# Kernel tuning notes

Measured on AMD Instinct MI355X. Metric: run time of the kernel, lower is better.

Reference implementation:

```python
import jax, jax.numpy as jnp
import numpy as np

B, D, H, G, WR = 8192, 1024, 1024, 2, 64
URANKS = [64, 64]


def setup_inputs() -> dict:
    key = jax.random.key(0)
    ks = jax.random.split(key, 12)
    s = 0.1
    return {
        "x": jax.random.normal(ks[0], (B, D), jnp.float32),
        "h": jax.random.normal(ks[1], (B, H), jnp.float32),
        "c": jax.random.normal(ks[2], (B, H), jnp.float32),
        "dia_x": s * jax.random.normal(ks[3], (1, D), jnp.float32),
        "dia_h": s * jax.random.normal(ks[4], (1, H), jnp.float32),
        "Ux": s * jax.random.normal(ks[5], (D, WR), jnp.float32),
        "Vx": s * jax.random.normal(ks[6], (4 * H, WR), jnp.float32),
        "Uh_0": s * jax.random.normal(ks[7], (G, H // G, URANKS[0]), jnp.float32),
        "Vh_0": s * jax.random.normal(ks[8], (G, URANKS[0], 4 * (H // G)), jnp.float32),
        "Uh_1": s * jax.random.normal(ks[9], (G, H // G, URANKS[1]), jnp.float32),
        "Vh_1": s * jax.random.normal(ks[10], (G, URANKS[1], 4 * (H // G)), jnp.float32),
        "bias_x": jnp.ones((1, 4 * H), jnp.float32),
        "bias_h": jnp.ones((1, 4 * H), jnp.float32),
    }


def reference(x, h, c, dia_x, dia_h, Ux, Vx, Uh_0, Vh_0, Uh_1, Vh_1, bias_x, bias_h):
    Bn, Dn = x.shape
    Hn = h.shape[1]
    g = Uh_0.shape[0]
    Hg = Hn // g
    r0 = Uh_0.shape[2]

    # diagonal (vector-multiplication) paths, x-part zero-padded to hidden width
    vm_x = jnp.pad(dia_x * x, ((0, 0), (0, Hn - Dn)))          # [B, H]
    vm_h = dia_h * h                                           # [B, H]

    # low-rank input projection
    lowered_x = (x @ Ux) @ Vx.T                                # [B, 4H]

    # refined diagonal corrections subtracted from the low-rank outputs
    Vx4 = Vx.reshape(4, Hn, -1)[:, :Dn, :]                     # [4, D, wR]
    coef_x = jnp.sum(Ux[None, :, :] * Vx4, axis=-1)            # [4, D]
    vm_refined_x = jnp.pad(x[:, None, :] * coef_x[None], ((0, 0), (0, 0), (0, Hn - Dn))).reshape(Bn, 4 * Hn)

    Uh0f = Uh_0.reshape(Hn, r0)                                # [H, r0]
    Vh0f = jnp.transpose(Vh_0, (0, 2, 1)).reshape(4 * Hn, r0).reshape(4, Hn, r0)
    coef_h = jnp.sum(Uh0f[None, :, :] * Vh0f, axis=-1)         # [4, H]
    vm_refined_h = (h[:, None, :] * coef_h[None]).reshape(Bn, 4 * Hn)

    gx = lowered_x - vm_refined_x + bias_x
    xi, xf, xo, xn = jnp.split(gx, 4, axis=1)

    # grouped low-rank recurrent projection with cyclic group permutation
    hv = h.reshape(Bn, g, Hg)
    Uhs = [Uh_0, Uh_1]
    Vhs = [Vh_0, Vh_1]
    g_h = jnp.zeros((Bn, 4 * Hn), x.dtype)
    for i in range(g):
        idx = np.roll(np.arange(g), -i)                        # static permutation
        hp = hv[:, idx, :]                                     # [B, g, H/g]
        t = jnp.einsum('bgn,gnr->bgr', hp, Uhs[i])             # [B, g, r_i]
        t = jnp.einsum('bgr,grm->bgm', t, Vhs[i])              # [B, g, 4H/g]
        g_h = g_h + t.reshape(Bn, 4 * Hn)

    gh = g_h - vm_refined_h + bias_h
    hf, hi, hn, ho = jnp.split(gh, 4, axis=1)                  # note gate order differs from x

    base = vm_x + vm_h
    inputgate = jax.nn.sigmoid(xi + hi + base)
    forgetgate = jax.nn.sigmoid(xf + hf + base)
    outputgate = jax.nn.sigmoid(xo + ho + base)
    newgate = jnp.tanh(xn + hn + base)

    c_next = forgetgate * c + inputgate * newgate
    h_next = outputgate * jnp.tanh(c_next)
    return (h_next, c_next)
```

## Files before the change

### kernel.cpp

```cpp
#include <hip/hip_runtime.h>


typedef _Float16 half8 __attribute__((ext_vector_type(8)));
typedef _Float16 half4v __attribute__((ext_vector_type(4)));
typedef float f32x4 __attribute__((ext_vector_type(4)));

#define WS_TA    0
#define WS_TB    3145728
#define WS_U1F   6291456
#define WS_UH1F  6422528
#define WS_W2    6684672
#define WS_CX    8257536
#define WS_CH    8273920
#define WS_BB    8290304

__global__ __launch_bounds__(256) void prep_kernel(
    const float* __restrict__ Ux, const float* __restrict__ Vx,
    const float* __restrict__ Uh0, const float* __restrict__ Vh0,
    const float* __restrict__ Uh1, const float* __restrict__ Vh1,
    const float* __restrict__ dia_x, const float* __restrict__ dia_h,
    const float* __restrict__ bias_x, const float* __restrict__ bias_h,
    _Float16* __restrict__ U1f, _Float16* __restrict__ Uh1f,
    _Float16* __restrict__ W2f, float* __restrict__ cx,
    float* __restrict__ ch, float* __restrict__ bb)
{
    int e = blockIdx.x * 256 + threadIdx.x;
    if (e < 8192) {
        int lane = e & 63, ks = (e >> 6) & 31, ct = e >> 11;
        int l15 = lane & 15, quad = lane >> 4;
        half8 v8;
        #pragma unroll
        for (int jj = 0; jj < 8; ++jj) {
            int k = ks * 32 + quad * 8 + jj;
            v8[jj] = (_Float16)Ux[k * 64 + ct * 16 + l15];
        }
        *(half8*)&U1f[(size_t)e * 8] = v8;
    } else if (e < 24576) {
        int t = e - 8192;
        int lane = t & 63, ks = (t >> 6) & 15, ct = (t >> 10) & 3, j = t >> 12;
        int l15 = lane & 15, quad = lane >> 4;
        const float* src = (j & 1) ? Uh1 : Uh0;
        int g = j >> 1;
        half8 v8;
        #pragma unroll
        for (int jj = 0; jj < 8; ++jj) {
            int k = ks * 32 + quad * 8 + jj;
            v8[jj] = (_Float16)src[(g * 512 + k) * 64 + ct * 16 + l15];
        }
        *(half8*)&Uh1f[(size_t)t * 8] = v8;
    } else if (e < 122880) {
        int t = e - 24576;
        int lane = t & 63;
        int ksq  = (t >> 6) % 6;
        int ct   = (t / 384) & 63;
        int g01  = (t / 24576) & 1;
        int s    = t / 49152;
        int l15 = lane & 15, quad = lane >> 4;
        int k = ct * 16 + l15;
        int jx = s * 2 + g01;
        int m = (g01 == 0) ? (1024 + k) : k;
        half8 v8;
        #pragma unroll
        for (int jj = 0; jj < 8; ++jj) {
            int kk = ksq * 32 + quad * 8 + jj;
            int r = kk & 63, sect = kk >> 6;
            float val;
            if (sect == 0)      val = Vx[(jx * 1024 + k) * 64 + r];
            else if (sect == 1) val = Vh0[(s * 64 + r) * 2048 + m];
            else                val = Vh1[(s * 64 + r) * 2048 + m];
            v8[jj] = (_Float16)val;
        }
        *(half8*)&W2f[(size_t)t * 8] = v8;
    } else if (e < 126976) {
        int t = e - 122880; int q = t >> 10; int k = t & 1023;
        int jh = q ^ 1;
        int fh = jh * 1024 + k; int g = fh >> 11; int m = fh & 2047;
        float sx = 0.f, sh = 0.f;
        for (int r = 0; r < 64; ++r) {
            sx += Ux[k * 64 + r] * Vx[(q * 1024 + k) * 64 + r];
            sh += Uh0[k * 64 + r] * Vh0[(g * 64 + r) * 2048 + m];
        }
        cx[t] = dia_x[k] - sx;
        ch[t] = dia_h[k] - sh;
        bb[t] = bias_x[q * 1024 + k] + bias_h[jh * 1024 + k];
    }
}

__global__ __launch_bounds__(256) void s1_kernel(
    const float* __restrict__ x, const float* __restrict__ h,
    const _Float16* __restrict__ U1f, const _Float16* __restrict__ Uh1f,
    _Float16* __restrict__ Ta, _Float16* __restrict__ Tb)
{
    __shared__ __align__(16) _Float16 Ash[16][520];

    const int job = blockIdx.y;
    const int b0 = blockIdx.x * 16;
    const int tid = threadIdx.x;
    const int w = tid >> 6, l = tid & 63, l15 = l & 15, quad = l >> 4;

    f32x4 acc0 = {}, acc1 = {};
    const int nkc = (job == 0) ? 2 : 1;
    const float* src = (job == 0) ? x : h;

    for (int kc = 0; kc < nkc; ++kc) {
        const int koff = (job == 2) ? 512 : kc * 512;
        #pragma unroll
        for (int ii = 0; ii < 8; ++ii) {
            int idx = tid + ii * 256;
            int row = idx >> 7, c4 = idx & 127;
            float4 f = *(const float4*)&src[(size_t)(b0 + row) * 1024 + koff + c4 * 4];
            half4v p;
            p[0] = (_Float16)f.x; p[1] = (_Float16)f.y;
            p[2] = (_Float16)f.z; p[3] = (_Float16)f.w;
            *(half4v*)&Ash[row][c4 * 4] = p;
        }
        __syncthreads();
        if (job == 0) {
            const _Float16* bp = U1f + ((size_t)(w * 32 + kc * 16) * 64 + l) * 8;
            #pragma unroll
            for (int ks = 0; ks < 16; ++ks) {
                half8 a = *(const half8*)&Ash[l15][ks * 32 + quad * 8];
                half8 b = *(const half8*)(bp + (size_t)ks * 512);
                acc0 = __builtin_amdgcn_mfma_f32_16x16x32_f16(a, b, acc0, 0, 0, 0);
            }
        } else {
            const int j0 = (job == 1) ? 0 : 1;
            const int j1 = (job == 1) ? 3 : 2;
            const _Float16* bp0 = Uh1f + ((size_t)((j0 * 4 + w) * 16) * 64 + l) * 8;
            const _Float16* bp1 = Uh1f + ((size_t)((j1 * 4 + w) * 16) * 64 + l) * 8;
            #pragma unroll
            for (int ks = 0; ks < 16; ++ks) {
                half8 a = *(const half8*)&Ash[l15][ks * 32 + quad * 8];
                half8 b0 = *(const half8*)(bp0 + (size_t)ks * 512);
                acc0 = __builtin_amdgcn_mfma_f32_16x16x32_f16(a, b0, acc0, 0, 0, 0);
                half8 b1 = *(const half8*)(bp1 + (size_t)ks * 512);
                acc1 = __builtin_amdgcn_mfma_f32_16x16x32_f16(a, b1, acc1, 0, 0, 0);
            }
        }
        __syncthreads();
    }
    if (job == 0) {
        int col = w * 16 + l15;
        #pragma unroll
        for (int r = 0; r < 4; ++r) {
            int row = b0 + quad * 4 + r;
            _Float16 v = (_Float16)acc0[r];
            Ta[(size_t)row * 192 + col] = v;
            Tb[(size_t)row * 192 + col] = v;
        }
    } else {
        int colA = ((job == 1) ? 64 : 128) + w * 16 + l15;
        int colB = ((job == 1) ? 128 : 64) + w * 16 + l15;
        #pragma unroll
        for (int r = 0; r < 4; ++r) {
            int row = b0 + quad * 4 + r;
            Ta[(size_t)row * 192 + colA] = (_Float16)acc0[r];
            Tb[(size_t)row * 192 + colB] = (_Float16)acc1[r];
        }
    }
}

__global__ __launch_bounds__(256, 4) void s2_kernel(
    const _Float16* __restrict__ Ta, const _Float16* __restrict__ Tb,
    const _Float16* __restrict__ W2f,
    const float* __restrict__ cx, const float* __restrict__ ch,
    const float* __restrict__ bb,
    const float* __restrict__ x, const float* __restrict__ h,
    const float* __restrict__ c, float* __restrict__ out)
{
    __shared__ __align__(16) _Float16 TaSh[32][200];
    __shared__ __align__(16) _Float16 TbSh[32][200];

    const int b0 = blockIdx.x * 32;
    const int by = blockIdx.y;
    const int tid = threadIdx.x;
    const int w = tid >> 6, l = tid & 63, l15 = l & 15, quad = l >> 4;

    #pragma unroll
    for (int ii = 0; ii < 6; ++ii) {
        int idx = tid + ii * 256;
        int arr = idx >= 768;
        int i2 = idx - (arr ? 768 : 0);
        int row = i2 / 24, c8 = i2 % 24;
        const _Float16* src = arr ? Tb : Ta;
        _Float16* dst = arr ? &TbSh[row][c8 * 8] : &TaSh[row][c8 * 8];
        *(half8*)dst = *(const half8*)&src[(size_t)(b0 + row) * 192 + c8 * 8];
    }
    __syncthreads();

    const size_t laneoff = (size_t)l * 8;

    #pragma unroll
    for (int kr = 0; kr < 2; ++kr) {
        const int ctg = by * 8 + kr * 4 + w;
        const int k = ctg * 16 + l15;
        f32x4 acc[4][2] = {};
        const _Float16* bpi = W2f + (size_t)((0 * 64 + ctg) * 6) * 512 + laneoff;
        const _Float16* bpf = W2f + (size_t)((1 * 64 + ctg) * 6) * 512 + laneoff;
        const _Float16* bpo = W2f + (size_t)((2 * 64 + ctg) * 6) * 512 + laneoff;
        const _Float16* bpn = W2f + (size_t)((3 * 64 + ctg) * 6) * 512 + laneoff;
        #pragma unroll
        for (int ks = 0; ks < 6; ++ks) {
            half8 bi = *(const half8*)(bpi + (size_t)ks * 512);
            half8 bf = *(const half8*)(bpf + (size_t)ks * 512);
            half8 bo = *(const half8*)(bpo + (size_t)ks * 512);
            half8 bn = *(const half8*)(bpn + (size_t)ks * 512);
            #pragma unroll
            for (int rt = 0; rt < 2; ++rt) {
                half8 aA = *(const half8*)&TaSh[rt * 16 + l15][ks * 32 + quad * 8];
                half8 aB = *(const half8*)&TbSh[rt * 16 + l15][ks * 32 + quad * 8];
                acc[0][rt] = __builtin_amdgcn_mfma_f32_16x16x32_f16(aA, bi, acc[0][rt], 0, 0, 0);
                acc[1][rt] = __builtin_amdgcn_mfma_f32_16x16x32_f16(aA, bf, acc[1][rt], 0, 0, 0);
                acc[2][rt] = __builtin_amdgcn_mfma_f32_16x16x32_f16(aB, bo, acc[2][rt], 0, 0, 0);
                acc[3][rt] = __builtin_amdgcn_mfma_f32_16x16x32_f16(aB, bn, acc[3][rt], 0, 0, 0);
            }
        }
        float cxi = cx[k], cxf = cx[1024 + k], cxo = cx[2048 + k], cxn = cx[3072 + k];
        float chi = ch[k], chf = ch[1024 + k], cho = ch[2048 + k], chn = ch[3072 + k];
        float bbi = bb[k], bbf = bb[1024 + k], bbo = bb[2048 + k], bbn = bb[3072 + k];
        #pragma unroll
        for (int rt = 0; rt < 2; ++rt) {
            #pragma unroll
            for (int r = 0; r < 4; ++r) {
                int row = b0 + rt * 16 + quad * 4 + r;
                size_t off = (size_t)row * 1024 + k;
                float xv = x[off], hv = h[off], cv = c[off];
                float pi = acc[0][rt][r] + xv * cxi + hv * chi + bbi;
                float pf = acc[1][rt][r] + xv * cxf + hv * chf + bbf;
                float po = acc[2][rt][r] + xv * cxo + hv * cho + bbo;
                float pn = acc[3][rt][r] + xv * cxn + hv * chn + bbn;
                float ig = __builtin_amdgcn_rcpf(1.f + __expf(-pi));
                float fg = __builtin_amdgcn_rcpf(1.f + __expf(-pf));
                float og = __builtin_amdgcn_rcpf(1.f + __expf(-po));
                float ng = 1.f - 2.f * __builtin_amdgcn_rcpf(__expf(2.f * pn) + 1.f);
                float cn = fg * cv + ig * ng;
                float tc = 1.f - 2.f * __builtin_amdgcn_rcpf(__expf(2.f * cn) + 1.f);
                out[off] = og * tc;
                out[(size_t)8388608 + off] = cn;
            }
        }
    }
}

extern "C" void kernel_launch(void* const* d_in, const int* in_sizes, int n_in,
                              void* d_out, int out_size, void* d_ws, size_t ws_size,
                              hipStream_t stream)
{
    const float* x      = (const float*)d_in[0];
    const float* h      = (const float*)d_in[1];
    const float* c      = (const float*)d_in[2];
    const float* dia_x  = (const float*)d_in[3];
    const float* dia_h  = (const float*)d_in[4];
    const float* Ux     = (const float*)d_in[5];
    const float* Vx     = (const float*)d_in[6];
    const float* Uh0    = (const float*)d_in[7];
    const float* Vh0    = (const float*)d_in[8];
    const float* Uh1    = (const float*)d_in[9];
    const float* Vh1    = (const float*)d_in[10];
    const float* bias_x = (const float*)d_in[11];
    const float* bias_h = (const float*)d_in[12];
    float* out = (float*)d_out;

    char* ws = (char*)d_ws;
    _Float16* TaW  = (_Float16*)(ws + WS_TA);
    _Float16* TbW  = (_Float16*)(ws + WS_TB);
    _Float16* U1f  = (_Float16*)(ws + WS_U1F);
    _Float16* Uh1f = (_Float16*)(ws + WS_UH1F);
    _Float16* W2f  = (_Float16*)(ws + WS_W2);
    float* cx = (float*)(ws + WS_CX);
    float* ch = (float*)(ws + WS_CH);
    float* bb = (float*)(ws + WS_BB);

    prep_kernel<<<496, 256, 0, stream>>>(Ux, Vx, Uh0, Vh0, Uh1, Vh1,
                                         dia_x, dia_h, bias_x, bias_h,
                                         U1f, Uh1f, W2f, cx, ch, bb);
    s1_kernel<<<dim3(512, 3), 256, 0, stream>>>(x, h, U1f, Uh1f, TaW, TbW);
    s2_kernel<<<dim3(256, 8), 256, 0, stream>>>(TaW, TbW, W2f, cx, ch, bb,
                                                x, h, c, out);
}
```

Baseline: 242.0 us.

## Parallelize coef reduction with wave shuffles; restructure s2 to drop LDS and prefetch

In prep_kernel, the 64-term coefficient dot products now use one thread per rank element, reduced across the wavefront with xor shuffles, instead of a serial loop per thread. The grid grows to match. In s2_kernel, the shared-memory staging of Ta/Tb and its barrier are removed: MFMA A operands are read straight from global memory. Each block now covers half as many gate columns (grid y doubled), and x/h/c plus the coefficient loads are issued before the MMA loop so their latency overlaps the matrix work. The trade-off is that Ta/Tb rows are re-read from global or L2 by more blocks, with more global A-operand traffic.

```diff
diff --git a/kernel.cpp b/kernel.cpp
--- a/kernel.cpp
+++ b/kernel.cpp
@@ -71,18 +71,25 @@
             v8[jj] = (_Float16)val;
         }
         *(half8*)&W2f[(size_t)t * 8] = v8;
-    } else if (e < 126976) {
-        int t = e - 122880; int q = t >> 10; int k = t & 1023;
+    } else {
+        int t64 = e - 122880;
+        int t = t64 >> 6;
+        int r = t64 & 63;
+        int q = t >> 10; int k = t & 1023;
         int jh = q ^ 1;
         int fh = jh * 1024 + k; int g = fh >> 11; int m = fh & 2047;
-        float sx = 0.f, sh = 0.f;
-        for (int r = 0; r < 64; ++r) {
-            sx += Ux[k * 64 + r] * Vx[(q * 1024 + k) * 64 + r];
-            sh += Uh0[k * 64 + r] * Vh0[(g * 64 + r) * 2048 + m];
-        }
-        cx[t] = dia_x[k] - sx;
-        ch[t] = dia_h[k] - sh;
-        bb[t] = bias_x[q * 1024 + k] + bias_h[jh * 1024 + k];
+        float sx = Ux[k * 64 + r] * Vx[(q * 1024 + k) * 64 + r];
+        float sh = Uh0[k * 64 + r] * Vh0[(g * 64 + r) * 2048 + m];
+        #pragma unroll
+        for (int d = 32; d > 0; d >>= 1) {
+            sx += __shfl_xor(sx, d, 64);
+            sh += __shfl_xor(sh, d, 64);
+        }
+        if (r == 0) {
+            cx[t] = dia_x[k] - sx;
+            ch[t] = dia_h[k] - sh;
+            bb[t] = bias_x[q * 1024 + k] + bias_h[jh * 1024 + k];
+        }
     }
 }
 
@@ -168,76 +175,71 @@
     const float* __restrict__ x, const float* __restrict__ h,
     const float* __restrict__ c, float* __restrict__ out)
 {
-    __shared__ __align__(16) _Float16 TaSh[32][200];
-    __shared__ __align__(16) _Float16 TbSh[32][200];
-
     const int b0 = blockIdx.x * 32;
-    const int by = blockIdx.y;
     const int tid = threadIdx.x;
     const int w = tid >> 6, l = tid & 63, l15 = l & 15, quad = l >> 4;
-
+    const int ctg = blockIdx.y * 4 + w;
+    const int k = ctg * 16 + l15;
+
+    const size_t base = (size_t)(b0 + quad * 4) * 1024 + k;
+    float xv[2][4], hv[2][4], cv[2][4];
     #pragma unroll
-    for (int ii = 0; ii < 6; ++ii) {
-        int idx = tid + ii * 256;
-        int arr = idx >= 768;
-        int i2 = idx - (arr ? 768 : 0);
-        int row = i2 / 24, c8 = i2 % 24;
-        const _Float16* src = arr ? Tb : Ta;
-        _Float16* dst = arr ? &TbSh[row][c8 * 8] : &TaSh[row][c8 * 8];
-        *(half8*)dst = *(const half8*)&src[(size_t)(b0 + row) * 192 + c8 * 8];
-    }
-    __syncthreads();
+    for (int rt = 0; rt < 2; ++rt) {
+        #pragma unroll
+        for (int r = 0; r < 4; ++r) {
+            size_t off = base + (size_t)(rt * 16 + r) * 1024;
+            xv[rt][r] = x[off];
+            hv[rt][r] = h[off];
+            cv[rt][r] = c[off];
+        }
+    }
+    float cxi = cx[k], cxf = cx[1024 + k], cxo = cx[2048 + k], cxn = cx[3072 + k];
+    float chi = ch[k], chf = ch[1024 + k], cho = ch[2048 + k], chn = ch[3072 + k];
+    float bbi = bb[k], bbf = bb[1024 + k], bbo = bb[2048 + k], bbn = bb[3072 + k];
 
     const size_t laneoff = (size_t)l * 8;
-
+    const _Float16* bpi = W2f + (size_t)((0 * 64 + ctg) * 6) * 512 + laneoff;
+    const _Float16* bpf = W2f + (size_t)((1 * 64 + ctg) * 6) * 512 + laneoff;
+    const _Float16* bpo = W2f + (size_t)((2 * 64 + ctg) * 6) * 512 + laneoff;
+    const _Float16* bpn = W2f + (size_t)((3 * 64 + ctg) * 6) * 512 + laneoff;
+    const _Float16* aTa = Ta + (size_t)(b0 + l15) * 192 + quad * 8;
+    const _Float16* aTb = Tb + (size_t)(b0 + l15) * 192 + quad * 8;
+
+    f32x4 acc[4][2] = {};
     #pragma unroll
-    for (int kr = 0; kr < 2; ++kr) {
-        const int ctg = by * 8 + kr * 4 + w;
-        const int k = ctg * 16 + l15;
-        f32x4 acc[4][2] = {};
-        const _Float16* bpi = W2f + (size_t)((0 * 64 + ctg) * 6) * 512 + laneoff;
-        const _Float16* bpf = W2f + (size_t)((1 * 64 + ctg) * 6) * 512 + laneoff;
-        const _Float16* bpo = W2f + (size_t)((2 * 64 + ctg) * 6) * 512 + laneoff;
-        const _Float16* bpn = W2f + (size_t)((3 * 64 + ctg) * 6) * 512 + laneoff;
-        #pragma unroll
-        for (int ks = 0; ks < 6; ++ks) {
-            half8 bi = *(const half8*)(bpi + (size_t)ks * 512);
-            half8 bf = *(const half8*)(bpf + (size_t)ks * 512);
-            half8 bo = *(const half8*)(bpo + (size_t)ks * 512);
-            half8 bn = *(const half8*)(bpn + (size_t)ks * 512);
-            #pragma unroll
-            for (int rt = 0; rt < 2; ++rt) {
-                half8 aA = *(const half8*)&TaSh[rt * 16 + l15][ks * 32 + quad * 8];
-                half8 aB = *(const half8*)&TbSh[rt * 16 + l15][ks * 32 + quad * 8];
-                acc[0][rt] = __builtin_amdgcn_mfma_f32_16x16x32_f16(aA, bi, acc[0][rt], 0, 0, 0);
-                acc[1][rt] = __builtin_amdgcn_mfma_f32_16x16x32_f16(aA, bf, acc[1][rt], 0, 0, 0);
-                acc[2][rt] = __builtin_amdgcn_mfma_f32_16x16x32_f16(aB, bo, acc[2][rt], 0, 0, 0);
-                acc[3][rt] = __builtin_amdgcn_mfma_f32_16x16x32_f16(aB, bn, acc[3][rt], 0, 0, 0);
-            }
-        }
-        float cxi = cx[k], cxf = cx[1024 + k], cxo = cx[2048 + k], cxn = cx[3072 + k];
-        float chi = ch[k], chf = ch[1024 + k], cho = ch[2048 + k], chn = ch[3072 + k];
-        float bbi = bb[k], bbf = bb[1024 + k], bbo = bb[2048 + k], bbn = bb[3072 + k];
+    for (int ks = 0; ks < 6; ++ks) {
+        half8 bi = *(const half8*)(bpi + (size_t)ks * 512);
+        half8 bf = *(const half8*)(bpf + (size_t)ks * 512);
+        half8 bo = *(const half8*)(bpo + (size_t)ks * 512);
+        half8 bn = *(const half8*)(bpn + (size_t)ks * 512);
         #pragma unroll
         for (int rt = 0; rt < 2; ++rt) {
-            #pragma unroll
-            for (int r = 0; r < 4; ++r) {
-                int row = b0 + rt * 16 + quad * 4 + r;
-                size_t off = (size_t)row * 1024 + k;
-                float xv = x[off], hv = h[off], cv = c[off];
-                float pi = acc[0][rt][r] + xv * cxi + hv * chi + bbi;
-                float pf = acc[1][rt][r] + xv * cxf + hv * chf + bbf;
-                float po = acc[2][rt][r] + xv * cxo + hv * cho + bbo;
-                float pn = acc[3][rt][r] + xv * cxn + hv * chn + bbn;
-                float ig = __builtin_amdgcn_rcpf(1.f + __expf(-pi));
-                float fg = __builtin_amdgcn_rcpf(1.f + __expf(-pf));
-                float og = __builtin_amdgcn_rcpf(1.f + __expf(-po));
-                float ng = 1.f - 2.f * __builtin_amdgcn_rcpf(__expf(2.f * pn) + 1.f);
-                float cn = fg * cv + ig * ng;
-                float tc = 1.f - 2.f * __builtin_amdgcn_rcpf(__expf(2.f * cn) + 1.f);
-                out[off] = og * tc;
-                out[(size_t)8388608 + off] = cn;
-            }
+            half8 aA = *(const half8*)(aTa + (size_t)(rt * 16) * 192 + ks * 32);
+            half8 aB = *(const half8*)(aTb + (size_t)(rt * 16) * 192 + ks * 32);
+            acc[0][rt] = __builtin_amdgcn_mfma_f32_16x16x32_f16(aA, bi, acc[0][rt], 0, 0, 0);
+            acc[1][rt] = __builtin_amdgcn_mfma_f32_16x16x32_f16(aA, bf, acc[1][rt], 0, 0, 0);
+            acc[2][rt] = __builtin_amdgcn_mfma_f32_16x16x32_f16(aB, bo, acc[2][rt], 0, 0, 0);
+            acc[3][rt] = __builtin_amdgcn_mfma_f32_16x16x32_f16(aB, bn, acc[3][rt], 0, 0, 0);
+        }
+    }
+
+    #pragma unroll
+    for (int rt = 0; rt < 2; ++rt) {
+        #pragma unroll
+        for (int r = 0; r < 4; ++r) {
+            size_t off = base + (size_t)(rt * 16 + r) * 1024;
+            float pi = acc[0][rt][r] + xv[rt][r] * cxi + hv[rt][r] * chi + bbi;
+            float pf = acc[1][rt][r] + xv[rt][r] * cxf + hv[rt][r] * chf + bbf;
+            float po = acc[2][rt][r] + xv[rt][r] * cxo + hv[rt][r] * cho + bbo;
+            float pn = acc[3][rt][r] + xv[rt][r] * cxn + hv[rt][r] * chn + bbn;
+            float ig = __builtin_amdgcn_rcpf(1.f + __expf(-pi));
+            float fg = __builtin_amdgcn_rcpf(1.f + __expf(-pf));
+            float og = __builtin_amdgcn_rcpf(1.f + __expf(-po));
+            float ng = 1.f - 2.f * __builtin_amdgcn_rcpf(__expf(2.f * pn) + 1.f);
+            float cn = fg * cv[rt][r] + ig * ng;
+            float tc = 1.f - 2.f * __builtin_amdgcn_rcpf(__expf(2.f * cn) + 1.f);
+            out[off] = og * tc;
+            out[(size_t)8388608 + off] = cn;
         }
     }
 }
@@ -271,10 +273,10 @@
     float* ch = (float*)(ws + WS_CH);
     float* bb = (float*)(ws + WS_BB);
 
-    prep_kernel<<<496, 256, 0, stream>>>(Ux, Vx, Uh0, Vh0, Uh1, Vh1,
-                                         dia_x, dia_h, bias_x, bias_h,
-                                         U1f, Uh1f, W2f, cx, ch, bb);
+    prep_kernel<<<1504, 256, 0, stream>>>(Ux, Vx, Uh0, Vh0, Uh1, Vh1,
+                                          dia_x, dia_h, bias_x, bias_h,
+                                          U1f, Uh1f, W2f, cx, ch, bb);
     s1_kernel<<<dim3(512, 3), 256, 0, stream>>>(x, h, U1f, Uh1f, TaW, TbW);
-    s2_kernel<<<dim3(256, 8), 256, 0, stream>>>(TaW, TbW, W2f, cx, ch, bb,
-                                                x, h, c, out);
-}
+    s2_kernel<<<dim3(256, 16), 256, 0, stream>>>(TaW, TbW, W2f, cx, ch, bb,
+                                                 x, h, c, out);
+}
```

Measured after the change: 257.6 us. +6.4%, slower.
